# Performance work log

Hardware: AMD Instinct MI355X
Metric: run time of the kernel (lower is better)

Reference implementation:

```python
import jax, jax.numpy as jnp
import numpy as np

C = 256; G = 16; GC = C // G; K = 3; P = K * K
N = 4; H = 64; W = 64
PAD = 1; OFFSET_SCALE = 1.0; LN_EPS = 1e-5


def setup_inputs() -> dict:
    key = jax.random.key(0)
    ks = jax.random.split(key, 8)
    s = 0.02
    return {
        "x": jax.random.normal(ks[0], (N, C, H, W), jnp.float32),
        "dw_w": jax.random.normal(ks[1], (C, 1, K, K), jnp.float32) * s,
        "dw_b": jnp.zeros((C,), jnp.float32),
        "ln_g": jnp.ones((C,), jnp.float32),
        "ln_b": jnp.zeros((C,), jnp.float32),
        "off_w": jax.random.normal(ks[2], (C, G * P * 2), jnp.float32) * s,
        "off_b": jnp.zeros((G * P * 2,), jnp.float32),
        "mask_w": jax.random.normal(ks[3], (C, G * P), jnp.float32) * s,
        "mask_b": jnp.zeros((G * P,), jnp.float32),
        "inp_w": jax.random.normal(ks[4], (C, C), jnp.float32) * s,
        "inp_b": jnp.zeros((C,), jnp.float32),
        "out_w": jax.random.normal(ks[5], (C, C), jnp.float32) * s,
        "out_b": jnp.zeros((C,), jnp.float32),
    }


def _dcnv3_nchw(x, dw_w, dw_b, ln_g, ln_b, off_w, off_b, mask_w, mask_b,
                inp_w, inp_b, out_w, out_b):
    # NCHW -> NHWC (wrapper permute)
    xn = jnp.transpose(x, (0, 2, 3, 1))                      # (N,H,W,C)
    x_proj = xn @ inp_w + inp_b                              # input_proj

    # offset/mask branch: depthwise conv (NCHW) -> LayerNorm (channels-last) -> GELU
    x1 = jax.lax.conv_general_dilated(
        x, dw_w, window_strides=(1, 1), padding=((PAD, PAD), (PAD, PAD)),
        dimension_numbers=("NCHW", "OIHW", "NCHW"), feature_group_count=C)
    x1 = jnp.transpose(x1, (0, 2, 3, 1)) + dw_b
    mu = x1.mean(-1, keepdims=True)
    var = ((x1 - mu) ** 2).mean(-1, keepdims=True)
    x1 = (x1 - mu) * jax.lax.rsqrt(var + LN_EPS) * ln_g + ln_b
    x1 = jax.nn.gelu(x1, approximate=False)

    offset = (x1 @ off_w + off_b).reshape(N, H, W, G, P, 2)  # (x,y) pairs
    mask = jax.nn.softmax((x1 @ mask_w + mask_b).reshape(N, H, W, G, P), axis=-1)

    # pad sampled feature map with zeros (F.pad before sampling)
    xp = jnp.pad(x_proj, ((0, 0), (PAD, PAD), (PAD, PAD), (0, 0)))
    Hin, Win = H + 2 * PAD, W + 2 * PAD
    xg = xp.reshape(N, Hin, Win, G, GC)

    # reference points, normalized by padded size
    ref_y = (jnp.arange(H, dtype=jnp.float32) + PAD + 0.5) / Hin
    ref_x = (jnp.arange(W, dtype=jnp.float32) + PAD + 0.5) / Win
    ref = jnp.stack([jnp.broadcast_to(ref_x[None, :], (H, W)),
                     jnp.broadcast_to(ref_y[:, None], (H, W))], -1)  # (H,W,2)

    # dilation grid: x varies in the outer loop (torch meshgrid 'ij')
    d = jnp.arange(K, dtype=jnp.float32) - (K - 1) // 2     # [-1,0,1]
    gx = jnp.repeat(d, K) / Win
    gy = jnp.tile(d, K) / Hin
    grid = jnp.stack([gx, gy], -1)                           # (P,2)

    norm = jnp.array([Win, Hin], jnp.float32)
    loc = (ref[None, :, :, None, None, :] + grid * OFFSET_SCALE
           + offset * OFFSET_SCALE / norm)                   # (N,H,W,G,P,2)

    # grid_sample bilinear, align_corners=False, zero padding
    px = loc[..., 0] * Win - 0.5
    py = loc[..., 1] * Hin - 0.5
    x0 = jnp.floor(px); y0 = jnp.floor(py)
    wx = px - x0; wy = py - y0
    x0i = x0.astype(jnp.int32); y0i = y0.astype(jnp.int32)

    n_idx = jnp.arange(N)[:, None, None, None, None]
    g_idx = jnp.arange(G)[None, None, None, :, None]

    def corner(iy, ix, w):
        valid = (iy >= 0) & (iy < Hin) & (ix >= 0) & (ix < Win)
        v = xg[n_idx, jnp.clip(iy, 0, Hin - 1), jnp.clip(ix, 0, Win - 1), g_idx]
        wgt = jnp.where(valid, w, 0.0) * mask                # fold mask into weights
        return jnp.einsum("nhwgp,nhwgpc->nhwgc", wgt, v)

    out = (corner(y0i, x0i, (1 - wy) * (1 - wx))
           + corner(y0i, x0i + 1, (1 - wy) * wx)
           + corner(y0i + 1, x0i, wy * (1 - wx))
           + corner(y0i + 1, x0i + 1, wy * wx))               # (N,H,W,G,GC)

    out = out.reshape(N, H, W, C) @ out_w + out_b            # output_proj
    return jnp.transpose(out, (0, 3, 1, 2))                  # NHWC -> NCHW


def reference(x, dw_w, dw_b, ln_g, ln_b, off_w, off_b, mask_w, mask_b,
              inp_w, inp_b, out_w, out_b):
    return _dcnv3_nchw(x, dw_w, dw_b, ln_g, ln_b, off_w, off_b,
                       mask_w, mask_b, inp_w, inp_b, out_w, out_b)
```

## Files before the change

### kernel.cpp

```cpp
#include <hip/hip_runtime.h>
#include <hip/hip_bf16.h>
#include <math.h>


using bf16x8 = __attribute__((ext_vector_type(8))) short;
using f32x4  = __attribute__((ext_vector_type(4))) float;

#define GLOBAL_AS __attribute__((address_space(1)))
#define LDS_AS    __attribute__((address_space(3)))

static __device__ inline void g2lds16(const void* g, void* l) {
  __builtin_amdgcn_global_load_lds((const GLOBAL_AS int*)g, (LDS_AS int*)l, 16, 0, 0);
}
static __device__ inline unsigned short f2bf(float v) {
  __hip_bfloat16 b = __float2bfloat16(v);
  return *reinterpret_cast<unsigned short*>(&b);
}
static __device__ inline float us2f(unsigned short u) {
  union { unsigned u; float f; } c; c.u = ((unsigned)u) << 16; return c.f;
}

__global__ __launch_bounds__(256) void prep_xt_k(
    const float* __restrict__ x,
    const float* __restrict__ inp_w, const float* __restrict__ off_w,
    const float* __restrict__ off_b, const float* __restrict__ mask_w,
    const float* __restrict__ mask_b, const float* __restrict__ out_w,
    __hip_bfloat16* __restrict__ BtI, __hip_bfloat16* __restrict__ BtOM,
    __hip_bfloat16* __restrict__ BtO, float* __restrict__ bOM,
    __hip_bfloat16* __restrict__ xT)
{
  __shared__ float tile[32][65];
  const int b = blockIdx.x, t = threadIdx.x;
  if (b < 1024) {
    if (b < 256) {
      int n = b;
      BtI[n * 256 + t] = __float2bfloat16(inp_w[t * 256 + n]);
    } else if (b < 768) {
      int n = b - 256;
      float v = 0.f;
      if (n < 288) v = off_w[t * 288 + n];
      else if (n < 432) v = mask_w[t * 144 + (n - 288)];
      BtOM[n * 256 + t] = __float2bfloat16(v);
      if (b == 256) {
        for (int idx = t; idx < 512; idx += 256) {
          float bv = (idx < 288) ? off_b[idx] : ((idx < 432) ? mask_b[idx - 288] : 0.f);
          bOM[idx] = bv;
        }
      }
    } else {
      int n = b - 768;
      BtO[n * 256 + t] = __float2bfloat16(out_w[t * 256 + n]);
    }
    return;
  }
  const int i = b - 1024;
  const int hw0 = (i & 63) * 64, c0 = ((i >> 6) & 7) * 32, n4 = i >> 9;
  #pragma unroll
  for (int r = 0; r < 8; ++r) {
    int idx = t + r * 256;
    int cl = idx >> 6, wl = idx & 63;
    tile[cl][wl] = x[(size_t)n4 * 1048576 + (size_t)(c0 + cl) * 4096 + hw0 + wl];
  }
  __syncthreads();
  #pragma unroll
  for (int r = 0; r < 2; ++r) {
    int idx = t + r * 256;
    int pixl = idx >> 3, cq = idx & 7;
    unsigned short b0 = f2bf(tile[cq * 4 + 0][pixl]);
    unsigned short b1 = f2bf(tile[cq * 4 + 1][pixl]);
    unsigned short b2 = f2bf(tile[cq * 4 + 2][pixl]);
    unsigned short b3 = f2bf(tile[cq * 4 + 3][pixl]);
    uint2 u;
    u.x = (unsigned)b0 | ((unsigned)b1 << 16);
    u.y = (unsigned)b2 | ((unsigned)b3 << 16);
    *(uint2*)&xT[((size_t)n4 * 4096 + hw0 + pixl) * 256 + c0 + cq * 4] = u;
  }
}

struct G64 {
  f32x4 acc[2][2];
  int wave, lane, quad, lr, wm, wn;
};

static __device__ inline void g64_loop(
    G64& g, const __hip_bfloat16* __restrict__ A,
    const __hip_bfloat16* __restrict__ Bt, size_t m0, int n0,
    short* As, short* Bs, int t)
{
  #pragma unroll
  for (int i = 0; i < 2; ++i)
    #pragma unroll
    for (int j = 0; j < 2; ++j)
      g.acc[i][j] = (f32x4){0.f, 0.f, 0.f, 0.f};
  const int row = t >> 2, kq = t & 3;
  for (int kt = 0; kt < 256; kt += 32) {
    g2lds16(A + (m0 + row) * 256 + kt + kq * 8, (char*)As + t * 16);
    g2lds16(Bt + (size_t)(n0 + row) * 256 + kt + kq * 8, (char*)Bs + t * 16);
    __syncthreads();
    bf16x8 bfv[2];
    #pragma unroll
    for (int ni = 0; ni < 2; ++ni)
      bfv[ni] = *(const bf16x8*)&Bs[(g.wn * 32 + ni * 16 + g.lr) * 32 + g.quad * 8];
    #pragma unroll
    for (int mi = 0; mi < 2; ++mi) {
      bf16x8 af = *(const bf16x8*)&As[(g.wm * 32 + mi * 16 + g.lr) * 32 + g.quad * 8];
      #pragma unroll
      for (int ni = 0; ni < 2; ++ni)
        g.acc[mi][ni] = __builtin_amdgcn_mfma_f32_16x16x32_bf16(af, bfv[ni], g.acc[mi][ni], 0, 0, 0);
    }
    __syncthreads();
  }
}

__global__ __launch_bounds__(256) void gemm_i(
    const __hip_bfloat16* __restrict__ xT, const __hip_bfloat16* __restrict__ BtI,
    const float* __restrict__ inp_b, __hip_bfloat16* __restrict__ xpu)
{
  __shared__ __align__(16) char smem[8192];
  short* As = (short*)smem;
  short* Bs = (short*)(smem + 4096);
  const int t = threadIdx.x;
  const int n0 = blockIdx.x * 64;
  const size_t m0 = (size_t)blockIdx.y * 64;

  G64 g;
  g.wave = t >> 6; g.lane = t & 63; g.quad = g.lane >> 4; g.lr = g.lane & 15;
  g.wm = g.wave >> 1; g.wn = g.wave & 1;
  g64_loop(g, xT, BtI, m0, n0, As, Bs, t);

  #pragma unroll
  for (int mi = 0; mi < 2; ++mi) {
    #pragma unroll
    for (int ni = 0; ni < 2; ++ni) {
      int col = n0 + g.wn * 32 + ni * 16 + g.lr;
      float bv = inp_b[col];
      #pragma unroll
      for (int reg = 0; reg < 4; ++reg) {
        size_t m = m0 + g.wm * 32 + mi * 16 + g.quad * 4 + reg;
        xpu[m * 256 + col] = __float2bfloat16(g.acc[mi][ni][reg] + bv);
      }
    }
  }
}

__global__ __launch_bounds__(1024) void stage2_k(
    const __hip_bfloat16* __restrict__ xT,
    const float* __restrict__ dw_w, const float* __restrict__ dw_b,
    const float* __restrict__ ln_g, const float* __restrict__ ln_b,
    const __hip_bfloat16* __restrict__ BtOM, const float* __restrict__ bOM,
    __hip_bfloat16* __restrict__ om)
{
  __shared__ __align__(16) char smem[62464];
  unsigned short* x1t = (unsigned short*)smem;
  unsigned short* xs  = (unsigned short*)(smem + 33792);
  float* wgt  = (float*)(smem + 33792 + 15360);
  float* psq  = (float*)(smem + 33792 + 15360 + 1152);
  float* murs = (float*)(smem + 33792 + 15360 + 1152 + 8192);
  short* Bs   = (short*)(smem + 33792);

  const int blk = blockIdx.x;
  const int n4 = blk >> 6, h = blk & 63;
  const int t = threadIdx.x;
  const int w = t & 63, q = t >> 6;

  float s1 = 0.f, s2 = 0.f;
  for (int chunk = 0; chunk < 8; ++chunk) {
    const int ch0 = chunk * 32;
    if (t < 768) {
      int r = t >> 8, i = t & 255;
      int px = i >> 2, cq = i & 3;
      int hh = h + r - 1;
      uint4 v = {0, 0, 0, 0};
      if ((unsigned)hh < 64u)
        v = *(const uint4*)(xT + ((size_t)n4 * 4096 + (size_t)hh * 64 + px) * 256 + ch0 + cq * 8);
      *(uint4*)&xs[(r * 64 + px) * 40 + cq * 8] = v;
    }
    if (t < 288) {
      int p = t >> 5, lc = t & 31;
      wgt[p * 32 + lc] = dw_w[(ch0 + lc) * 9 + p];
    }
    __syncthreads();
    {
      int c = ch0 + 2 * q;
      float a0 = dw_b[c], a1 = dw_b[c + 1];
      #pragma unroll
      for (int p = 0; p < 9; ++p) {
        int dh = p / 3, dwd = p % 3 - 1;
        int ww = w + dwd;
        if ((unsigned)ww < 64u) {
          unsigned xv = *(const unsigned*)&xs[(dh * 64 + ww) * 40 + 2 * q];
          float wa = wgt[p * 32 + 2 * q], wb = wgt[p * 32 + 2 * q + 1];
          a0 = fmaf(us2f((unsigned short)(xv & 0xffff)), wa, a0);
          a1 = fmaf(us2f((unsigned short)(xv >> 16)), wb, a1);
        }
      }
      s1 += a0 + a1;
      s2 = fmaf(a0, a0, fmaf(a1, a1, s2));
      unsigned pk = (unsigned)f2bf(a0) | ((unsigned)f2bf(a1) << 16);
      *(unsigned*)&x1t[w * 264 + c] = pk;
    }
    __syncthreads();
  }

  psq[q * 64 + w] = s1;
  psq[1024 + q * 64 + w] = s2;
  __syncthreads();
  if (t < 64) {
    float a = 0.f, b = 0.f;
    #pragma unroll
    for (int j = 0; j < 16; ++j) { a += psq[j * 64 + t]; b += psq[1024 + j * 64 + t]; }
    float mu = a * (1.f / 256.f);
    murs[t] = mu;
    murs[64 + t] = rsqrtf(b * (1.f / 256.f) - mu * mu + 1e-5f);
  }
  __syncthreads();
  {
    float mu = murs[w], rs = murs[64 + w];
    #pragma unroll
    for (int chunk = 0; chunk < 8; ++chunk) {
      int c = chunk * 32 + 2 * q;
      unsigned pk = *(const unsigned*)&x1t[w * 264 + c];
      float v0 = us2f((unsigned short)(pk & 0xffff));
      float v1 = us2f((unsigned short)(pk >> 16));
      float y0 = fmaf((v0 - mu) * rs, ln_g[c], ln_b[c]);
      float y1 = fmaf((v1 - mu) * rs, ln_g[c + 1], ln_b[c + 1]);
      float g0 = 0.5f * y0 * (1.f + erff(y0 * 0.70710678f));
      float g1 = 0.5f * y1 * (1.f + erff(y1 * 0.70710678f));
      *(unsigned*)&x1t[w * 264 + c] = (unsigned)f2bf(g0) | ((unsigned)f2bf(g1) << 16);
    }
  }
  __syncthreads();

  const int wave = t >> 6, lane = t & 63;
  const int quad = lane >> 4, lr = lane & 15;
  const int wm = wave >> 2, wn = wave & 3;
  f32x4 acc[7];
  #pragma unroll
  for (int i = 0; i < 7; ++i) acc[i] = (f32x4){0.f, 0.f, 0.f, 0.f};

  for (int kt = 0; kt < 256; kt += 32) {
    __syncthreads();
    {
      int col = t >> 2, kq = t & 3;
      g2lds16(BtOM + (size_t)col * 256 + kt + kq * 8, (char*)Bs + t * 16);
      int j = t + 1024;
      if (j < 1792) {
        col = j >> 2; kq = j & 3;
        g2lds16(BtOM + (size_t)col * 256 + kt + kq * 8, (char*)Bs + j * 16);
      }
    }
    __syncthreads();
    bf16x8 af = *(const bf16x8*)&x1t[(wm * 16 + lr) * 264 + kt + quad * 8];
    #pragma unroll
    for (int ni = 0; ni < 7; ++ni) {
      bf16x8 bf = *(const bf16x8*)&Bs[(wn * 112 + ni * 16 + lr) * 32 + quad * 8];
      acc[ni] = __builtin_amdgcn_mfma_f32_16x16x32_bf16(af, bf, acc[ni], 0, 0, 0);
    }
  }

  const size_t pix0 = (size_t)n4 * 4096 + (size_t)h * 64;
  #pragma unroll
  for (int ni = 0; ni < 7; ++ni) {
    int col = wn * 112 + ni * 16 + lr;
    if (col < 432) {
      float bv = bOM[col];
      #pragma unroll
      for (int reg = 0; reg < 4; ++reg) {
        int m = wm * 16 + quad * 4 + reg;
        om[(pix0 + m) * 448 + col] = __float2bfloat16(acc[ni][reg] + bv);
      }
    }
  }
}

__global__ __launch_bounds__(256) void sample_k(
    const __hip_bfloat16* __restrict__ xpu, const __hip_bfloat16* __restrict__ om,
    __hip_bfloat16* __restrict__ samp)
{
  __shared__ unsigned short oms[16 * 448];
  const int bid = blockIdx.x;
  const int region = bid & 7;
  const int q = bid >> 3;
  const int pix0 = region * 2048 + q * 16;
  const int t = threadIdx.x;

  {
    const uint4* gsrc = (const uint4*)(om + (size_t)pix0 * 448);
    uint4* ldst = (uint4*)oms;
    #pragma unroll
    for (int r = 0; r < 4; ++r) {
      int i = t + r * 256;
      if (i < 896) ldst[i] = gsrc[i];
    }
  }
  __syncthreads();

  const int g = t & 15;
  const int pl = t >> 4;
  const int pix = pix0 + pl;
  const int n4 = pix >> 12;
  const int hw = pix & 4095;
  const int h = hw >> 6, w = hw & 63;

  float mk[9];
  {
    const unsigned short* mp = &oms[pl * 448 + 288 + g * 9];
    float mx = -1e30f;
    #pragma unroll
    for (int p = 0; p < 9; ++p) { mk[p] = us2f(mp[p]); mx = fmaxf(mx, mk[p]); }
    float se = 0.f;
    #pragma unroll
    for (int p = 0; p < 9; ++p) { mk[p] = __expf(mk[p] - mx); se += mk[p]; }
    float inv = 1.f / se;
    #pragma unroll
    for (int p = 0; p < 9; ++p) mk[p] *= inv;
  }

  const unsigned short* op = &oms[pl * 448 + g * 18];
  const __hip_bfloat16* xpg = xpu + (g << 4);
  float ax[16];
  #pragma unroll
  for (int i = 0; i < 16; ++i) ax[i] = 0.f;

  auto corner = [&](int iy, int ix, float wt) {
    if ((unsigned)(iy - 1) >= 64u || (unsigned)(ix - 1) >= 64u) return;
    const __hip_bfloat16* src =
        xpg + ((size_t)((n4 << 12) + (iy - 1) * 64 + (ix - 1)) << 8);
    uint4 u0 = *(const uint4*)src;
    uint4 u1 = *(const uint4*)(src + 8);
    const unsigned uu[8] = {u0.x, u0.y, u0.z, u0.w, u1.x, u1.y, u1.z, u1.w};
    #pragma unroll
    for (int i = 0; i < 8; ++i) {
      float lo = us2f((unsigned short)(uu[i] & 0xffff));
      float hi = us2f((unsigned short)(uu[i] >> 16));
      ax[2 * i + 0] = fmaf(wt, lo, ax[2 * i + 0]);
      ax[2 * i + 1] = fmaf(wt, hi, ax[2 * i + 1]);
    }
  };

  #pragma unroll
  for (int p = 0; p < 9; ++p) {
    float ox = us2f(op[2 * p]), oy = us2f(op[2 * p + 1]);
    float px = (float)(w + p / 3) + ox;
    float py = (float)(h + p % 3) + oy;
    float xf = floorf(px), yf = floorf(py);
    float wx = px - xf, wy = py - yf;
    int ix = (int)xf, iy = (int)yf;
    float m = mk[p];
    corner(iy,     ix,     (1.f - wy) * (1.f - wx) * m);
    corner(iy,     ix + 1, (1.f - wy) * wx * m);
    corner(iy + 1, ix,     wy * (1.f - wx) * m);
    corner(iy + 1, ix + 1, wy * wx * m);
  }

  unsigned short ub[16];
  #pragma unroll
  for (int i = 0; i < 16; ++i) ub[i] = f2bf(ax[i]);
  uint4* d4 = (uint4*)(samp + (size_t)pix * 256 + (g << 4));
  uint4 u0, u1;
  u0.x = (unsigned)ub[0] | ((unsigned)ub[1] << 16);
  u0.y = (unsigned)ub[2] | ((unsigned)ub[3] << 16);
  u0.z = (unsigned)ub[4] | ((unsigned)ub[5] << 16);
  u0.w = (unsigned)ub[6] | ((unsigned)ub[7] << 16);
  u1.x = (unsigned)ub[8] | ((unsigned)ub[9] << 16);
  u1.y = (unsigned)ub[10] | ((unsigned)ub[11] << 16);
  u1.z = (unsigned)ub[12] | ((unsigned)ub[13] << 16);
  u1.w = (unsigned)ub[14] | ((unsigned)ub[15] << 16);
  d4[0] = u0; d4[1] = u1;
}

__global__ __launch_bounds__(256) void gemm_o(
    const __hip_bfloat16* __restrict__ samp, const __hip_bfloat16* __restrict__ BtO,
    const float* __restrict__ out_b, float* __restrict__ out)
{
  __shared__ __align__(16) char smem[8448];
  short* As = (short*)smem;
  short* Bs = (short*)(smem + 4096);
  float* tb = (float*)smem;
  const int t = threadIdx.x;
  const int n0 = blockIdx.x * 64;
  const size_t m0 = (size_t)blockIdx.y * 64;

  G64 g;
  g.wave = t >> 6; g.lane = t & 63; g.quad = g.lane >> 4; g.lr = g.lane & 15;
  g.wm = g.wave >> 1; g.wn = g.wave & 1;
  g64_loop(g, samp, BtO, m0, n0, As, Bs, t);

  const int n4 = (int)(m0 >> 12), hw0 = (int)(m0 & 4095);
  for (int qc = 0; qc < 2; ++qc) {
    __syncthreads();
    if (g.wn == qc) {
      #pragma unroll
      for (int ni = 0; ni < 2; ++ni) {
        int cl = ni * 16 + g.lr;
        float bv = out_b[n0 + qc * 32 + cl];
        #pragma unroll
        for (int mi = 0; mi < 2; ++mi)
          #pragma unroll
          for (int reg = 0; reg < 4; ++reg)
            tb[cl * 65 + g.wm * 32 + mi * 16 + g.quad * 4 + reg] =
                g.acc[mi][ni][reg] + bv;
      }
    }
    __syncthreads();
    #pragma unroll
    for (int r = 0; r < 2; ++r) {
      int idx = t + r * 256;
      int row = idx >> 4, mc = (idx & 15) * 4;
      int co = n0 + qc * 32 + row;
      float4 v;
      v.x = tb[row * 65 + mc + 0];
      v.y = tb[row * 65 + mc + 1];
      v.z = tb[row * 65 + mc + 2];
      v.w = tb[row * 65 + mc + 3];
      *(float4*)&out[(size_t)(n4 * 256 + co) * 4096 + hw0 + mc] = v;
    }
  }
}

extern "C" void kernel_launch(void* const* d_in, const int* in_sizes, int n_in,
                              void* d_out, int out_size, void* d_ws, size_t ws_size,
                              hipStream_t stream) {
  const float* x      = (const float*)d_in[0];
  const float* dw_w   = (const float*)d_in[1];
  const float* dw_b   = (const float*)d_in[2];
  const float* ln_g   = (const float*)d_in[3];
  const float* ln_b   = (const float*)d_in[4];
  const float* off_w  = (const float*)d_in[5];
  const float* off_b  = (const float*)d_in[6];
  const float* mask_w = (const float*)d_in[7];
  const float* mask_b = (const float*)d_in[8];
  const float* inp_w  = (const float*)d_in[9];
  const float* inp_b  = (const float*)d_in[10];
  const float* out_w  = (const float*)d_in[11];
  const float* out_b  = (const float*)d_in[12];
  float* out = (float*)d_out;

  char* w0 = (char*)d_ws;
  __hip_bfloat16* xpu  = (__hip_bfloat16*)(w0);
  __hip_bfloat16* xT   = (__hip_bfloat16*)(w0 + 8388608);
  __hip_bfloat16* samp = xT;
  __hip_bfloat16* om   = (__hip_bfloat16*)(w0 + 16777216);
  __hip_bfloat16* BtI  = (__hip_bfloat16*)(w0 + 31457280);
  __hip_bfloat16* BtOM = (__hip_bfloat16*)(w0 + 31588352);
  __hip_bfloat16* BtO  = (__hip_bfloat16*)(w0 + 31850496);
  float*          bOM  = (float*)(w0 + 31981568);
  if (ws_size < 31983616) return;

  prep_xt_k<<<3072, 256, 0, stream>>>(x, inp_w, off_w, off_b, mask_w, mask_b,
                                      out_w, BtI, BtOM, BtO, bOM, xT);
  gemm_i<<<dim3(4, 256), 256, 0, stream>>>(xT, BtI, inp_b, xpu);
  stage2_k<<<256, 1024, 0, stream>>>(xT, dw_w, dw_b, ln_g, ln_b, BtOM, bOM, om);
  sample_k<<<1024, 256, 0, stream>>>(xpu, om, samp);
  gemm_o<<<dim3(4, 256), 256, 0, stream>>>(samp, BtO, out_b, out);
}
```

Before: 163.3 us.

## Drop NHWC transpose pass and fuse sampling with output projection GEMM

Removes the x-to-bf16 NHWC transpose kernel. gemm_i and the depthwise-conv stage now read the fp32 NCHW input directly and convert it to bf16 in LDS. The sampling kernel is fused with the output projection: each block keeps its 16 sampled pixels in LDS and runs the 256-wide GEMM against BtO. This saves the samp round trip through global memory and one launch. The cost is that every sampling block reloads the full BtO weight slice, uses a 16-row MFMA tile, and gemm_i does more scalar LDS conversion work.

Result: slower. 170.4 us (+4.3%).

```diff
diff --git a/kernel.cpp b/kernel.cpp
--- a/kernel.cpp
+++ b/kernel.cpp
@@ -20,131 +20,104 @@
   union { unsigned u; float f; } c; c.u = ((unsigned)u) << 16; return c.f;
 }
 
-__global__ __launch_bounds__(256) void prep_xt_k(
-    const float* __restrict__ x,
+__global__ __launch_bounds__(256) void prep_k(
     const float* __restrict__ inp_w, const float* __restrict__ off_w,
     const float* __restrict__ off_b, const float* __restrict__ mask_w,
     const float* __restrict__ mask_b, const float* __restrict__ out_w,
     __hip_bfloat16* __restrict__ BtI, __hip_bfloat16* __restrict__ BtOM,
-    __hip_bfloat16* __restrict__ BtO, float* __restrict__ bOM,
-    __hip_bfloat16* __restrict__ xT)
+    __hip_bfloat16* __restrict__ BtO, float* __restrict__ bOM)
 {
-  __shared__ float tile[32][65];
-  const int b = blockIdx.x, t = threadIdx.x;
-  if (b < 1024) {
-    if (b < 256) {
-      int n = b;
-      BtI[n * 256 + t] = __float2bfloat16(inp_w[t * 256 + n]);
-    } else if (b < 768) {
-      int n = b - 256;
-      float v = 0.f;
-      if (n < 288) v = off_w[t * 288 + n];
-      else if (n < 432) v = mask_w[t * 144 + (n - 288)];
-      BtOM[n * 256 + t] = __float2bfloat16(v);
-      if (b == 256) {
-        for (int idx = t; idx < 512; idx += 256) {
-          float bv = (idx < 288) ? off_b[idx] : ((idx < 432) ? mask_b[idx - 288] : 0.f);
-          bOM[idx] = bv;
-        }
-      }
-    } else {
-      int n = b - 768;
-      BtO[n * 256 + t] = __float2bfloat16(out_w[t * 256 + n]);
-    }
-    return;
-  }
-  const int i = b - 1024;
-  const int hw0 = (i & 63) * 64, c0 = ((i >> 6) & 7) * 32, n4 = i >> 9;
-  #pragma unroll
-  for (int r = 0; r < 8; ++r) {
-    int idx = t + r * 256;
-    int cl = idx >> 6, wl = idx & 63;
-    tile[cl][wl] = x[(size_t)n4 * 1048576 + (size_t)(c0 + cl) * 4096 + hw0 + wl];
-  }
-  __syncthreads();
-  #pragma unroll
-  for (int r = 0; r < 2; ++r) {
-    int idx = t + r * 256;
-    int pixl = idx >> 3, cq = idx & 7;
-    unsigned short b0 = f2bf(tile[cq * 4 + 0][pixl]);
-    unsigned short b1 = f2bf(tile[cq * 4 + 1][pixl]);
-    unsigned short b2 = f2bf(tile[cq * 4 + 2][pixl]);
-    unsigned short b3 = f2bf(tile[cq * 4 + 3][pixl]);
-    uint2 u;
-    u.x = (unsigned)b0 | ((unsigned)b1 << 16);
-    u.y = (unsigned)b2 | ((unsigned)b3 << 16);
-    *(uint2*)&xT[((size_t)n4 * 4096 + hw0 + pixl) * 256 + c0 + cq * 4] = u;
-  }
-}
-
-struct G64 {
-  f32x4 acc[2][2];
-  int wave, lane, quad, lr, wm, wn;
-};
-
-static __device__ inline void g64_loop(
-    G64& g, const __hip_bfloat16* __restrict__ A,
-    const __hip_bfloat16* __restrict__ Bt, size_t m0, int n0,
-    short* As, short* Bs, int t)
-{
-  #pragma unroll
-  for (int i = 0; i < 2; ++i)
-    #pragma unroll
-    for (int j = 0; j < 2; ++j)
-      g.acc[i][j] = (f32x4){0.f, 0.f, 0.f, 0.f};
-  const int row = t >> 2, kq = t & 3;
-  for (int kt = 0; kt < 256; kt += 32) {
-    g2lds16(A + (m0 + row) * 256 + kt + kq * 8, (char*)As + t * 16);
-    g2lds16(Bt + (size_t)(n0 + row) * 256 + kt + kq * 8, (char*)Bs + t * 16);
-    __syncthreads();
-    bf16x8 bfv[2];
-    #pragma unroll
-    for (int ni = 0; ni < 2; ++ni)
-      bfv[ni] = *(const bf16x8*)&Bs[(g.wn * 32 + ni * 16 + g.lr) * 32 + g.quad * 8];
-    #pragma unroll
-    for (int mi = 0; mi < 2; ++mi) {
-      bf16x8 af = *(const bf16x8*)&As[(g.wm * 32 + mi * 16 + g.lr) * 32 + g.quad * 8];
-      #pragma unroll
-      for (int ni = 0; ni < 2; ++ni)
-        g.acc[mi][ni] = __builtin_amdgcn_mfma_f32_16x16x32_bf16(af, bfv[ni], g.acc[mi][ni], 0, 0, 0);
-    }
-    __syncthreads();
+  int b = blockIdx.x, t = threadIdx.x;
+  if (b < 256) {
+    int n = b;
+    BtI[n * 256 + t] = __float2bfloat16(inp_w[t * 256 + n]);
+  } else if (b < 768) {
+    int n = b - 256;
+    float v = 0.f;
+    if (n < 288) v = off_w[t * 288 + n];
+    else if (n < 432) v = mask_w[t * 144 + (n - 288)];
+    BtOM[n * 256 + t] = __float2bfloat16(v);
+    if (b == 256) {
+      for (int idx = t; idx < 512; idx += 256) {
+        float bv = (idx < 288) ? off_b[idx] : ((idx < 432) ? mask_b[idx - 288] : 0.f);
+        bOM[idx] = bv;
+      }
+    }
+  } else {
+    int n = b - 768;
+    BtO[n * 256 + t] = __float2bfloat16(out_w[t * 256 + n]);
   }
 }
 
 __global__ __launch_bounds__(256) void gemm_i(
-    const __hip_bfloat16* __restrict__ xT, const __hip_bfloat16* __restrict__ BtI,
+    const float* __restrict__ x, const __hip_bfloat16* __restrict__ BtI,
     const float* __restrict__ inp_b, __hip_bfloat16* __restrict__ xpu)
 {
-  __shared__ __align__(16) char smem[8192];
-  short* As = (short*)smem;
-  short* Bs = (short*)(smem + 4096);
+  __shared__ __align__(16) char smem[12288];
+  float* Asf = (float*)smem;
+  short* Bs  = (short*)(smem + 8192);
   const int t = threadIdx.x;
   const int n0 = blockIdx.x * 64;
   const size_t m0 = (size_t)blockIdx.y * 64;
-
-  G64 g;
-  g.wave = t >> 6; g.lane = t & 63; g.quad = g.lane >> 4; g.lr = g.lane & 15;
-  g.wm = g.wave >> 1; g.wn = g.wave & 1;
-  g64_loop(g, xT, BtI, m0, n0, As, Bs, t);
+  const int n4 = (int)(m0 >> 12), hw0 = (int)(m0 & 4095);
+
+  const int wave = t >> 6, lane = t & 63;
+  const int quad = lane >> 4, lr = lane & 15;
+  const int wm = wave >> 1, wn = wave & 1;
+
+  f32x4 acc[2][2];
+  #pragma unroll
+  for (int i = 0; i < 2; ++i)
+    #pragma unroll
+    for (int j = 0; j < 2; ++j)
+      acc[i][j] = (f32x4){0.f, 0.f, 0.f, 0.f};
+
+  for (int kt = 0; kt < 256; kt += 32) {
+    #pragma unroll
+    for (int j = 0; j < 2; ++j) {
+      int idx = j * 256 + t;
+      int kk = idx >> 4, px4 = (idx & 15) * 4;
+      g2lds16(x + (size_t)n4 * 1048576 + (size_t)(kt + kk) * 4096 + hw0 + px4,
+              (char*)Asf + idx * 16);
+    }
+    g2lds16(BtI + (size_t)(n0 + (t >> 2)) * 256 + kt + (t & 3) * 8,
+            (char*)Bs + t * 16);
+    __syncthreads();
+    bf16x8 bfv[2];
+    #pragma unroll
+    for (int ni = 0; ni < 2; ++ni)
+      bfv[ni] = *(const bf16x8*)&Bs[(wn * 32 + ni * 16 + lr) * 32 + quad * 8];
+    #pragma unroll
+    for (int mi = 0; mi < 2; ++mi) {
+      int m = wm * 32 + mi * 16 + lr;
+      bf16x8 af;
+      #pragma unroll
+      for (int j2 = 0; j2 < 8; ++j2)
+        ((unsigned short*)&af)[j2] = f2bf(Asf[(quad * 8 + j2) * 64 + m]);
+      #pragma unroll
+      for (int ni = 0; ni < 2; ++ni)
+        acc[mi][ni] = __builtin_amdgcn_mfma_f32_16x16x32_bf16(af, bfv[ni], acc[mi][ni], 0, 0, 0);
+    }
+    __syncthreads();
+  }
 
   #pragma unroll
   for (int mi = 0; mi < 2; ++mi) {
     #pragma unroll
     for (int ni = 0; ni < 2; ++ni) {
-      int col = n0 + g.wn * 32 + ni * 16 + g.lr;
+      int col = n0 + wn * 32 + ni * 16 + lr;
       float bv = inp_b[col];
       #pragma unroll
       for (int reg = 0; reg < 4; ++reg) {
-        size_t m = m0 + g.wm * 32 + mi * 16 + g.quad * 4 + reg;
-        xpu[m * 256 + col] = __float2bfloat16(g.acc[mi][ni][reg] + bv);
+        size_t m = m0 + wm * 32 + mi * 16 + quad * 4 + reg;
+        xpu[m * 256 + col] = __float2bfloat16(acc[mi][ni][reg] + bv);
       }
     }
   }
 }
 
 __global__ __launch_bounds__(1024) void stage2_k(
-    const __hip_bfloat16* __restrict__ xT,
+    const float* __restrict__ x,
     const float* __restrict__ dw_w, const float* __restrict__ dw_b,
     const float* __restrict__ ln_g, const float* __restrict__ ln_b,
     const __hip_bfloat16* __restrict__ BtOM, const float* __restrict__ bOM,
@@ -153,9 +126,9 @@
   __shared__ __align__(16) char smem[62464];
   unsigned short* x1t = (unsigned short*)smem;
   unsigned short* xs  = (unsigned short*)(smem + 33792);
-  float* wgt  = (float*)(smem + 33792 + 15360);
-  float* psq  = (float*)(smem + 33792 + 15360 + 1152);
-  float* murs = (float*)(smem + 33792 + 15360 + 1152 + 8192);
+  float* wgt  = (float*)(smem + 33792 + 13824);
+  float* psq  = (float*)(smem + 33792 + 13824 + 1152);
+  float* murs = (float*)(smem + 33792 + 13824 + 1152 + 8192);
   short* Bs   = (short*)(smem + 33792);
 
   const int blk = blockIdx.x;
@@ -167,13 +140,22 @@
   for (int chunk = 0; chunk < 8; ++chunk) {
     const int ch0 = chunk * 32;
     if (t < 768) {
-      int r = t >> 8, i = t & 255;
-      int px = i >> 2, cq = i & 3;
+      int seg = t >> 3, part = t & 7;
+      int r = seg >> 5, c = seg & 31;
+      int px0 = part * 8;
       int hh = h + r - 1;
-      uint4 v = {0, 0, 0, 0};
-      if ((unsigned)hh < 64u)
-        v = *(const uint4*)(xT + ((size_t)n4 * 4096 + (size_t)hh * 64 + px) * 256 + ch0 + cq * 8);
-      *(uint4*)&xs[(r * 64 + px) * 40 + cq * 8] = v;
+      float4 v0 = {0,0,0,0}, v1 = {0,0,0,0};
+      if ((unsigned)hh < 64u) {
+        const float* src = x + (size_t)n4 * 1048576 + (size_t)(ch0 + c) * 4096 + hh * 64 + px0;
+        v0 = *(const float4*)src;
+        v1 = *(const float4*)(src + 4);
+      }
+      uint4 u;
+      u.x = (unsigned)f2bf(v0.x) | ((unsigned)f2bf(v0.y) << 16);
+      u.y = (unsigned)f2bf(v0.z) | ((unsigned)f2bf(v0.w) << 16);
+      u.z = (unsigned)f2bf(v1.x) | ((unsigned)f2bf(v1.y) << 16);
+      u.w = (unsigned)f2bf(v1.z) | ((unsigned)f2bf(v1.w) << 16);
+      *(uint4*)&xs[(r * 32 + c) * 72 + px0] = u;
     }
     if (t < 288) {
       int p = t >> 5, lc = t & 31;
@@ -181,23 +163,22 @@
     }
     __syncthreads();
     {
-      int c = ch0 + 2 * q;
+      int lc = 2 * q;
+      int c = ch0 + lc;
       float a0 = dw_b[c], a1 = dw_b[c + 1];
       #pragma unroll
       for (int p = 0; p < 9; ++p) {
         int dh = p / 3, dwd = p % 3 - 1;
         int ww = w + dwd;
         if ((unsigned)ww < 64u) {
-          unsigned xv = *(const unsigned*)&xs[(dh * 64 + ww) * 40 + 2 * q];
-          float wa = wgt[p * 32 + 2 * q], wb = wgt[p * 32 + 2 * q + 1];
-          a0 = fmaf(us2f((unsigned short)(xv & 0xffff)), wa, a0);
-          a1 = fmaf(us2f((unsigned short)(xv >> 16)), wb, a1);
+          float wa = wgt[p * 32 + lc], wb = wgt[p * 32 + lc + 1];
+          a0 = fmaf(us2f(xs[(dh * 32 + lc) * 72 + ww]), wa, a0);
+          a1 = fmaf(us2f(xs[(dh * 32 + lc + 1) * 72 + ww]), wb, a1);
         }
       }
       s1 += a0 + a1;
       s2 = fmaf(a0, a0, fmaf(a1, a1, s2));
-      unsigned pk = (unsigned)f2bf(a0) | ((unsigned)f2bf(a1) << 16);
-      *(unsigned*)&x1t[w * 264 + c] = pk;
+      *(unsigned*)&x1t[w * 264 + c] = (unsigned)f2bf(a0) | ((unsigned)f2bf(a1) << 16);
     }
     __syncthreads();
   }
@@ -229,7 +210,6 @@
       *(unsigned*)&x1t[w * 264 + c] = (unsigned)f2bf(g0) | ((unsigned)f2bf(g1) << 16);
     }
   }
-  __syncthreads();
 
   const int wave = t >> 6, lane = t & 63;
   const int quad = lane >> 4, lr = lane & 15;
@@ -273,15 +253,22 @@
   }
 }
 
-__global__ __launch_bounds__(256) void sample_k(
+__global__ __launch_bounds__(256) void samp_o(
     const __hip_bfloat16* __restrict__ xpu, const __hip_bfloat16* __restrict__ om,
-    __hip_bfloat16* __restrict__ samp)
+    const __hip_bfloat16* __restrict__ BtO, const float* __restrict__ out_b,
+    float* __restrict__ out)
 {
-  __shared__ unsigned short oms[16 * 448];
+  __shared__ __align__(16) char smem[39168];
+  unsigned short* oms   = (unsigned short*)smem;
+  unsigned short* sampS = (unsigned short*)(smem + 14336);
+  short* Bs = (short*)(smem + 22784);
+  float* tb = (float*)smem;
+
   const int bid = blockIdx.x;
   const int region = bid & 7;
-  const int q = bid >> 3;
-  const int pix0 = region * 2048 + q * 16;
+  const int qb = bid >> 3;
+  const int pix0 = region * 2048 + qb * 16;
+  const int n4 = pix0 >> 12, hw0 = pix0 & 4095;
   const int t = threadIdx.x;
 
   {
@@ -295,15 +282,13 @@
   }
   __syncthreads();
 
-  const int g = t & 15;
-  const int pl = t >> 4;
-  const int pix = pix0 + pl;
-  const int n4 = pix >> 12;
-  const int hw = pix & 4095;
-  const int h = hw >> 6, w = hw & 63;
-
-  float mk[9];
   {
+    const int g = t & 15;
+    const int pl = t >> 4;
+    const int hw = hw0 + pl;
+    const int h = hw >> 6, w = hw & 63;
+
+    float mk[9];
     const unsigned short* mp = &oms[pl * 448 + 288 + g * 9];
     float mx = -1e30f;
     #pragma unroll
@@ -314,106 +299,106 @@
     float inv = 1.f / se;
     #pragma unroll
     for (int p = 0; p < 9; ++p) mk[p] *= inv;
-  }
-
-  const unsigned short* op = &oms[pl * 448 + g * 18];
-  const __hip_bfloat16* xpg = xpu + (g << 4);
-  float ax[16];
-  #pragma unroll
-  for (int i = 0; i < 16; ++i) ax[i] = 0.f;
-
-  auto corner = [&](int iy, int ix, float wt) {
-    if ((unsigned)(iy - 1) >= 64u || (unsigned)(ix - 1) >= 64u) return;
-    const __hip_bfloat16* src =
-        xpg + ((size_t)((n4 << 12) + (iy - 1) * 64 + (ix - 1)) << 8);
-    uint4 u0 = *(const uint4*)src;
-    uint4 u1 = *(const uint4*)(src + 8);
-    const unsigned uu[8] = {u0.x, u0.y, u0.z, u0.w, u1.x, u1.y, u1.z, u1.w};
-    #pragma unroll
-    for (int i = 0; i < 8; ++i) {
-      float lo = us2f((unsigned short)(uu[i] & 0xffff));
-      float hi = us2f((unsigned short)(uu[i] >> 16));
-      ax[2 * i + 0] = fmaf(wt, lo, ax[2 * i + 0]);
-      ax[2 * i + 1] = fmaf(wt, hi, ax[2 * i + 1]);
-    }
-  };
-
-  #pragma unroll
-  for (int p = 0; p < 9; ++p) {
-    float ox = us2f(op[2 * p]), oy = us2f(op[2 * p + 1]);
-    float px = (float)(w + p / 3) + ox;
-    float py = (float)(h + p % 3) + oy;
-    float xf = floorf(px), yf = floorf(py);
-    float wx = px - xf, wy = py - yf;
-    int ix = (int)xf, iy = (int)yf;
-    float m = mk[p];
-    corner(iy,     ix,     (1.f - wy) * (1.f - wx) * m);
-    corner(iy,     ix + 1, (1.f - wy) * wx * m);
-    corner(iy + 1, ix,     wy * (1.f - wx) * m);
-    corner(iy + 1, ix + 1, wy * wx * m);
-  }
-
-  unsigned short ub[16];
-  #pragma unroll
-  for (int i = 0; i < 16; ++i) ub[i] = f2bf(ax[i]);
-  uint4* d4 = (uint4*)(samp + (size_t)pix * 256 + (g << 4));
-  uint4 u0, u1;
-  u0.x = (unsigned)ub[0] | ((unsigned)ub[1] << 16);
-  u0.y = (unsigned)ub[2] | ((unsigned)ub[3] << 16);
-  u0.z = (unsigned)ub[4] | ((unsigned)ub[5] << 16);
-  u0.w = (unsigned)ub[6] | ((unsigned)ub[7] << 16);
-  u1.x = (unsigned)ub[8] | ((unsigned)ub[9] << 16);
-  u1.y = (unsigned)ub[10] | ((unsigned)ub[11] << 16);
-  u1.z = (unsigned)ub[12] | ((unsigned)ub[13] << 16);
-  u1.w = (unsigned)ub[14] | ((unsigned)ub[15] << 16);
-  d4[0] = u0; d4[1] = u1;
-}
-
-__global__ __launch_bounds__(256) void gemm_o(
-    const __hip_bfloat16* __restrict__ samp, const __hip_bfloat16* __restrict__ BtO,
-    const float* __restrict__ out_b, float* __restrict__ out)
-{
-  __shared__ __align__(16) char smem[8448];
-  short* As = (short*)smem;
-  short* Bs = (short*)(smem + 4096);
-  float* tb = (float*)smem;
-  const int t = threadIdx.x;
-  const int n0 = blockIdx.x * 64;
-  const size_t m0 = (size_t)blockIdx.y * 64;
-
-  G64 g;
-  g.wave = t >> 6; g.lane = t & 63; g.quad = g.lane >> 4; g.lr = g.lane & 15;
-  g.wm = g.wave >> 1; g.wn = g.wave & 1;
-  g64_loop(g, samp, BtO, m0, n0, As, Bs, t);
-
-  const int n4 = (int)(m0 >> 12), hw0 = (int)(m0 & 4095);
-  for (int qc = 0; qc < 2; ++qc) {
-    __syncthreads();
-    if (g.wn == qc) {
-      #pragma unroll
-      for (int ni = 0; ni < 2; ++ni) {
-        int cl = ni * 16 + g.lr;
-        float bv = out_b[n0 + qc * 32 + cl];
-        #pragma unroll
-        for (int mi = 0; mi < 2; ++mi)
-          #pragma unroll
-          for (int reg = 0; reg < 4; ++reg)
-            tb[cl * 65 + g.wm * 32 + mi * 16 + g.quad * 4 + reg] =
-                g.acc[mi][ni][reg] + bv;
-      }
-    }
-    __syncthreads();
-    #pragma unroll
-    for (int r = 0; r < 2; ++r) {
-      int idx = t + r * 256;
-      int row = idx >> 4, mc = (idx & 15) * 4;
-      int co = n0 + qc * 32 + row;
+
+    const unsigned short* op = &oms[pl * 448 + g * 18];
+    const __hip_bfloat16* xpg = xpu + (g << 4);
+    float ax[16];
+    #pragma unroll
+    for (int i = 0; i < 16; ++i) ax[i] = 0.f;
+
+    auto corner = [&](int iy, int ix, float wt) {
+      if ((unsigned)(iy - 1) >= 64u || (unsigned)(ix - 1) >= 64u) return;
+      const __hip_bfloat16* src =
+          xpg + ((size_t)((n4 << 12) + (iy - 1) * 64 + (ix - 1)) << 8);
+      uint4 u0 = *(const uint4*)src;
+      uint4 u1 = *(const uint4*)(src + 8);
+      const unsigned uu[8] = {u0.x, u0.y, u0.z, u0.w, u1.x, u1.y, u1.z, u1.w};
+      #pragma unroll
+      for (int i = 0; i < 8; ++i) {
+        float lo = us2f((unsigned short)(uu[i] & 0xffff));
+        float hi = us2f((unsigned short)(uu[i] >> 16));
+        ax[2 * i + 0] = fmaf(wt, lo, ax[2 * i + 0]);
+        ax[2 * i + 1] = fmaf(wt, hi, ax[2 * i + 1]);
+      }
+    };
+
+    #pragma unroll
+    for (int p = 0; p < 9; ++p) {
+      float ox = us2f(op[2 * p]), oy = us2f(op[2 * p + 1]);
+      float px = (float)(w + p / 3) + ox;
+      float py = (float)(h + p % 3) + oy;
+      float xf = floorf(px), yf = floorf(py);
+      float wx = px - xf, wy = py - yf;
+      int ix = (int)xf, iy = (int)yf;
+      float m = mk[p];
+      corner(iy,     ix,     (1.f - wy) * (1.f - wx) * m);
+      corner(iy,     ix + 1, (1.f - wy) * wx * m);
+      corner(iy + 1, ix,     wy * (1.f - wx) * m);
+      corner(iy + 1, ix + 1, wy * wx * m);
+    }
+
+    unsigned short ub[16];
+    #pragma unroll
+    for (int i = 0; i < 16; ++i) ub[i] = f2bf(ax[i]);
+    uint4 u0, u1;
+    u0.x = (unsigned)ub[0] | ((unsigned)ub[1] << 16);
+    u0.y = (unsigned)ub[2] | ((unsigned)ub[3] << 16);
+    u0.z = (unsigned)ub[4] | ((unsigned)ub[5] << 16);
+    u0.w = (unsigned)ub[6] | ((unsigned)ub[7] << 16);
+    u1.x = (unsigned)ub[8] | ((unsigned)ub[9] << 16);
+    u1.y = (unsigned)ub[10] | ((unsigned)ub[11] << 16);
+    u1.z = (unsigned)ub[12] | ((unsigned)ub[13] << 16);
+    u1.w = (unsigned)ub[14] | ((unsigned)ub[15] << 16);
+    *(uint4*)&sampS[pl * 264 + g * 16] = u0;
+    *(uint4*)&sampS[pl * 264 + g * 16 + 8] = u1;
+  }
+  __syncthreads();
+
+  const int wave = t >> 6, lane = t & 63;
+  const int quad = lane >> 4, lr = lane & 15;
+  f32x4 acc[4];
+  #pragma unroll
+  for (int i = 0; i < 4; ++i) acc[i] = (f32x4){0.f, 0.f, 0.f, 0.f};
+
+  for (int kt = 0; kt < 256; kt += 32) {
+    if (kt) __syncthreads();
+    #pragma unroll
+    for (int j = 0; j < 4; ++j) {
+      int idx = j * 256 + t;
+      int col = idx >> 2, kq = idx & 3;
+      g2lds16(BtO + (size_t)col * 256 + kt + kq * 8, (char*)Bs + idx * 16);
+    }
+    __syncthreads();
+    bf16x8 af = *(const bf16x8*)&sampS[lr * 264 + kt + quad * 8];
+    #pragma unroll
+    for (int ni = 0; ni < 4; ++ni) {
+      bf16x8 bf = *(const bf16x8*)&Bs[(wave * 64 + ni * 16 + lr) * 32 + quad * 8];
+      acc[ni] = __builtin_amdgcn_mfma_f32_16x16x32_bf16(af, bf, acc[ni], 0, 0, 0);
+    }
+  }
+  __syncthreads();
+
+  #pragma unroll
+  for (int ni = 0; ni < 4; ++ni) {
+    int col = wave * 64 + ni * 16 + lr;
+    float bv = out_b[col];
+    #pragma unroll
+    for (int reg = 0; reg < 4; ++reg)
+      tb[col * 17 + quad * 4 + reg] = acc[ni][reg] + bv;
+  }
+  __syncthreads();
+
+  {
+    int co = t;
+    float* dst = out + (size_t)(n4 * 256 + co) * 4096 + hw0;
+    #pragma unroll
+    for (int j = 0; j < 4; ++j) {
       float4 v;
-      v.x = tb[row * 65 + mc + 0];
-      v.y = tb[row * 65 + mc + 1];
-      v.z = tb[row * 65 + mc + 2];
-      v.w = tb[row * 65 + mc + 3];
-      *(float4*)&out[(size_t)(n4 * 256 + co) * 4096 + hw0 + mc] = v;
+      v.x = tb[co * 17 + j * 4 + 0];
+      v.y = tb[co * 17 + j * 4 + 1];
+      v.z = tb[co * 17 + j * 4 + 2];
+      v.w = tb[co * 17 + j * 4 + 3];
+      *(float4*)(dst + j * 4) = v;
     }
   }
 }
@@ -438,19 +423,16 @@
 
   char* w0 = (char*)d_ws;
   __hip_bfloat16* xpu  = (__hip_bfloat16*)(w0);
-  __hip_bfloat16* xT   = (__hip_bfloat16*)(w0 + 8388608);
-  __hip_bfloat16* samp = xT;
-  __hip_bfloat16* om   = (__hip_bfloat16*)(w0 + 16777216);
-  __hip_bfloat16* BtI  = (__hip_bfloat16*)(w0 + 31457280);
-  __hip_bfloat16* BtOM = (__hip_bfloat16*)(w0 + 31588352);
-  __hip_bfloat16* BtO  = (__hip_bfloat16*)(w0 + 31850496);
-  float*          bOM  = (float*)(w0 + 31981568);
-  if (ws_size < 31983616) return;
-
-  prep_xt_k<<<3072, 256, 0, stream>>>(x, inp_w, off_w, off_b, mask_w, mask_b,
-                                      out_w, BtI, BtOM, BtO, bOM, xT);
-  gemm_i<<<dim3(4, 256), 256, 0, stream>>>(xT, BtI, inp_b, xpu);
-  stage2_k<<<256, 1024, 0, stream>>>(xT, dw_w, dw_b, ln_g, ln_b, BtOM, bOM, om);
-  sample_k<<<1024, 256, 0, stream>>>(xpu, om, samp);
-  gemm_o<<<dim3(4, 256), 256, 0, stream>>>(samp, BtO, out_b, out);
-}
+  __hip_bfloat16* om   = (__hip_bfloat16*)(w0 + 8388608);
+  __hip_bfloat16* BtI  = (__hip_bfloat16*)(w0 + 23068672);
+  __hip_bfloat16* BtOM = (__hip_bfloat16*)(w0 + 23199744);
+  __hip_bfloat16* BtO  = (__hip_bfloat16*)(w0 + 23461888);
+  float*          bOM  = (float*)(w0 + 23592960);
+  if (ws_size < 23595008) return;
+
+  prep_k<<<1024, 256, 0, stream>>>(inp_w, off_w, off_b, mask_w, mask_b, out_w,
+                                   BtI, BtOM, BtO, bOM);
+  gemm_i<<<dim3(4, 256), 256, 0, stream>>>(x, BtI, inp_b, xpu);
+  stage2_k<<<256, 1024, 0, stream>>>(x, dw_w, dw_b, ln_g, ln_b, BtOM, bOM, om);
+  samp_o<<<1024, 256, 0, stream>>>(xpu, om, BtO, out_b, out);
+}
```
